# Performance work log

Measured on AMD Instinct MI355X. Metric: run time of the kernel, lower is better.

Reference implementation:

```python
import jax, jax.numpy as jnp
import numpy as np

B, T, C = 2, 1024, 1024
E, F, K = 8, 2048, 2


def setup_inputs() -> dict:
    key = jax.random.key(0)
    ks = jax.random.split(key, 5)
    s = 1.0 / np.sqrt(C)
    return {
        "x": jax.random.normal(ks[0], (B, T, C), jnp.float32),
        "Wr": jax.random.normal(ks[1], (E, C), jnp.float32) * s,   # router weight [E, d_model]
        "w1": jax.random.normal(ks[2], (E, C, F), jnp.float32) * s, # gate proj per expert
        "w3": jax.random.normal(ks[3], (E, C, F), jnp.float32) * s, # up proj per expert
        "w2": jax.random.normal(ks[4], (E, F, C), jnp.float32) * (1.0 / np.sqrt(F)),  # down proj
    }


def reference(x, Wr, w1, w3, w2):
    Bq, Tq, Cq = x.shape
    flat = x.reshape(-1, Cq)                          # [N, C]
    N = flat.shape[0]
    probs = jax.nn.softmax(flat @ Wr.T, axis=-1)      # [N, E]
    topw, topi = jax.lax.top_k(probs, K)              # [N, K]
    topw = topw / jnp.sum(topw, axis=-1, keepdims=True)
    # dense gate matrix: zero for unselected experts (same math as masked loop)
    gates = jnp.zeros((N, E), flat.dtype).at[jnp.arange(N)[:, None], topi].set(topw)
    # evaluate all experts, weight by gates (gate=0 kills unrouted experts)
    h1 = jnp.einsum('nd,edf->nef', flat, w1)          # [N, E, F]
    h3 = jnp.einsum('nd,edf->nef', flat, w3)
    h = jax.nn.silu(h1) * h3
    y = jnp.einsum('nef,efd->ned', h, w2)             # [N, E, C]
    out = jnp.einsum('ned,ne->nd', y, gates)          # [N, C]
    return out.reshape(Bq, Tq, Cq)
```

## Files before the change

### kernel.cpp

```cpp
#include <hip/hip_runtime.h>
#include <math.h>

typedef _Float16 f16;
typedef _Float16 f16x2 __attribute__((ext_vector_type(2)));
typedef _Float16 f16x4 __attribute__((ext_vector_type(4)));
typedef _Float16 f16x8 __attribute__((ext_vector_type(8)));
typedef __fp16 h16x2 __attribute__((ext_vector_type(2)));
typedef float f32x4 __attribute__((ext_vector_type(4)));
typedef float f32x16 __attribute__((ext_vector_type(16)));

#define N_TOK 2048
#define C_DIM 1024
#define E_NUM 8
#define F_DIM 2048
#define BM 256

#define WS_COUNTS    0
#define WS_OFFSETS   64
#define WS_CURSOR    192
#define WS_TOPI      256
#define WS_TOPW      (WS_TOPI + 16384)
#define WS_ROWS      (WS_TOPW + 16384)
#define WS_SLOT      (WS_ROWS + 16384)
#define WS_X16       (1ull << 20)
#define WS_H         (6ull << 20)
#define WS_Y0        (23ull << 20)
#define WS_Y1        (32ull << 20)

__device__ __forceinline__ f16x2 pkrtz(float a, float b) {
  union { h16x2 h; f16x2 f; } u;
  u.h = __builtin_amdgcn_cvt_pkrtz(a, b);
  return u.f;
}

__global__ void cvtx_kernel(const float* __restrict__ x, f16* __restrict__ x16) {
  int i = (blockIdx.x * 256 + threadIdx.x) * 8;
  f32x4 a = *(const f32x4*)(x + i);
  f32x4 b = *(const f32x4*)(x + i + 4);
  union { f16x8 v; f16x2 h[4]; } u;
  u.h[0] = pkrtz(a[0], a[1]);
  u.h[1] = pkrtz(a[2], a[3]);
  u.h[2] = pkrtz(b[0], b[1]);
  u.h[3] = pkrtz(b[2], b[3]);
  *(f16x8*)(x16 + i) = u.v;
}

__global__ void router_kernel(const float* __restrict__ x, const float* __restrict__ Wr,
                              int* counts, int* topi, float* topw) {
  int tok = blockIdx.x * 4 + (threadIdx.x >> 6);
  int lane = threadIdx.x & 63;
  const float* xr = x + (size_t)tok * C_DIM;
  float xv[16];
#pragma unroll
  for (int i = 0; i < 16; ++i) xv[i] = xr[i * 64 + lane];
  float logit[E_NUM];
#pragma unroll
  for (int e = 0; e < E_NUM; ++e) {
    const float* wr = Wr + (size_t)e * C_DIM;
    float acc = 0.f;
#pragma unroll
    for (int i = 0; i < 16; ++i) acc += xv[i] * wr[i * 64 + lane];
#pragma unroll
    for (int s = 1; s < 64; s <<= 1) acc += __shfl_xor(acc, s, 64);
    logit[e] = acc;
  }
  if (lane == 0) {
    float m = logit[0];
#pragma unroll
    for (int e = 1; e < E_NUM; ++e) m = fmaxf(m, logit[e]);
    float p[E_NUM];
#pragma unroll
    for (int e = 0; e < E_NUM; ++e) p[e] = expf(logit[e] - m);
    float p0 = -1.f, p1 = -1.f;
    int i0 = 0, i1 = 0;
#pragma unroll
    for (int e = 0; e < E_NUM; ++e) {
      float v = p[e];
      if (v > p0) { p1 = p0; i1 = i0; p0 = v; i0 = e; }
      else if (v > p1) { p1 = v; i1 = e; }
    }
    float inv = 1.f / (p0 + p1);
    topi[2 * tok] = i0; topi[2 * tok + 1] = i1;
    topw[2 * tok] = p0 * inv; topw[2 * tok + 1] = p1 * inv;
    atomicAdd(&counts[i0], 1);
    atomicAdd(&counts[i1], 1);
  }
}

__global__ void scan_kernel(const int* counts, int* offsets, int* cursor) {
  if (threadIdx.x == 0) {
    int o = 0;
    for (int e = 0; e < E_NUM; ++e) {
      offsets[e] = o; cursor[e] = o;
      o += counts[e];
    }
    offsets[E_NUM] = o;
  }
}

__global__ void scatter_kernel(const int* __restrict__ topi, int* cursor,
                               int* rows_perm, int* slot_of) {
  int n = blockIdx.x * blockDim.x + threadIdx.x;
  if (n >= N_TOK) return;
#pragma unroll
  for (int k = 0; k < 2; ++k) {
    int e = topi[2 * n + k];
    int pos = atomicAdd(&cursor[e], 1);
    rows_perm[pos] = n;
    slot_of[2 * n + k] = pos;
  }
}

#define BARRIER_PUB()                                          \
  asm volatile("s_waitcnt lgkmcnt(0)" ::: "memory");           \
  __builtin_amdgcn_s_barrier();                                \
  asm volatile("" ::: "memory");

#define UP_PACK_WRITE()                                                  \
  { union { f16x8 v; f16x2 h[4]; } u;                                    \
    u.h[0] = pkrtz(b1r[0], b1r[1]); u.h[1] = pkrtz(b1r[2], b1r[3]);      \
    u.h[2] = pkrtz(b1r[4], b1r[5]); u.h[3] = pkrtz(b1r[6], b1r[7]);      \
    *(f16x8*)&B1_lds[cur][bso] = u.v;                                    \
    u.h[0] = pkrtz(b3r[0], b3r[1]); u.h[1] = pkrtz(b3r[2], b3r[3]);      \
    u.h[2] = pkrtz(b3r[4], b3r[5]); u.h[3] = pkrtz(b3r[6], b3r[7]);      \
    *(f16x8*)&B3_lds[cur][bso] = u.v; }

#define UP_LOAD(ANXT, KN)                                                \
  { _Pragma("unroll") for (int j = 0; j < 8; ++j) {                      \
      b1r[j] = w1p[(size_t)(KN + j) * F_DIM];                            \
      b3r[j] = w3p[(size_t)(KN + j) * F_DIM]; }                          \
    _Pragma("unroll") for (int mi = 0; mi < 2; ++mi)                     \
      _Pragma("unroll") for (int kk = 0; kk < 2; ++kk)                   \
        ANXT[mi][kk] = *(const f16x8*)(aptr[mi] + (KN) + kk * 16 + fh * 8); }

#define UP_MFMA(ACUR)                                                    \
  { f16x8 bf[2][2];                                                      \
    _Pragma("unroll") for (int ni = 0; ni < 2; ++ni)                     \
      _Pragma("unroll") for (int kk = 0; kk < 2; ++kk) {                 \
        int col = wc + ni * 32 + ln31;                                   \
        int cell = (kk * 2 + fh) ^ ((col >> 1) & 3);                     \
        bf[ni][kk] = *(const f16x8*)&B1_lds[cur][col * 32 + cell * 8]; } \
    __builtin_amdgcn_s_setprio(1);                                       \
    _Pragma("unroll") for (int kk = 0; kk < 2; ++kk)                     \
      _Pragma("unroll") for (int mi = 0; mi < 2; ++mi)                   \
        _Pragma("unroll") for (int ni = 0; ni < 2; ++ni)                 \
          acc1[mi][ni] = __builtin_amdgcn_mfma_f32_32x32x16_f16(ACUR[mi][kk], bf[ni][kk], acc1[mi][ni], 0, 0, 0); \
    __builtin_amdgcn_s_setprio(0);                                       \
    _Pragma("unroll") for (int ni = 0; ni < 2; ++ni)                     \
      _Pragma("unroll") for (int kk = 0; kk < 2; ++kk) {                 \
        int col = wc + ni * 32 + ln31;                                   \
        int cell = (kk * 2 + fh) ^ ((col >> 1) & 3);                     \
        bf[ni][kk] = *(const f16x8*)&B3_lds[cur][col * 32 + cell * 8]; } \
    __builtin_amdgcn_s_setprio(1);                                       \
    _Pragma("unroll") for (int kk = 0; kk < 2; ++kk)                     \
      _Pragma("unroll") for (int mi = 0; mi < 2; ++mi)                   \
        _Pragma("unroll") for (int ni = 0; ni < 2; ++ni)                 \
          acc3[mi][ni] = __builtin_amdgcn_mfma_f32_32x32x16_f16(ACUR[mi][kk], bf[ni][kk], acc3[mi][ni], 0, 0, 0); \
    __builtin_amdgcn_s_setprio(0);                                       \
    cur ^= 1; }

#define UP_STEP(ACUR, ANXT, KN) \
  { UP_PACK_WRITE(); UP_LOAD(ANXT, KN); BARRIER_PUB(); UP_MFMA(ACUR); }

__launch_bounds__(512, 2)
__global__ void upproj_kernel(const f16* __restrict__ x16,
                              const float* __restrict__ w1,
                              const float* __restrict__ w3,
                              const int* __restrict__ counts,
                              const int* __restrict__ offsets,
                              const int* __restrict__ rows_perm,
                              f16* __restrict__ h_buf) {
  __shared__ __align__(16) f16 B1_lds[2][128 * 32];
  __shared__ __align__(16) f16 B3_lds[2][128 * 32];

  int bid = blockIdx.x;
  int e = bid & 7;
  int slot = bid >> 3;
  int fidx = slot & 15;
  int tile = slot >> 4;
  int cnt = counts[e];
  if (tile * BM >= cnt) return;
  int row0 = tile * BM;
  int off = offsets[e];
  int f0 = fidx * 128;
  int t = threadIdx.x, wid = t >> 6, lane = t & 63;
  int ln31 = lane & 31, fh = lane >> 5;
  int wr = (wid >> 1) * 64, wc = (wid & 1) * 64;

  const f16* aptr[2];
#pragma unroll
  for (int mi = 0; mi < 2; ++mi) {
    int lr = row0 + wr + mi * 32 + ln31;
    if (lr > cnt - 1) lr = cnt - 1;
    aptr[mi] = x16 + (size_t)rows_perm[off + lr] * C_DIM;
  }

  int bcol = t & 127, kg = t >> 7;
  int bso = bcol * 32 + ((kg ^ ((bcol >> 1) & 3)) * 8);
  const size_t eb = (size_t)e * C_DIM * F_DIM;
  const float* w1p = w1 + eb + (size_t)(kg * 8) * F_DIM + f0 + bcol;
  const float* w3p = w3 + eb + (size_t)(kg * 8) * F_DIM + f0 + bcol;

  f32x16 acc1[2][2] = {};
  f32x16 acc3[2][2] = {};
  float b1r[8], b3r[8];
  f16x8 aX[2][2], aY[2][2];
  int cur = 0;

  UP_LOAD(aX, 0);
  for (int tp = 0; tp < 15; ++tp) {
    UP_STEP(aX, aY, (2 * tp + 1) * 32);
    UP_STEP(aY, aX, (2 * tp + 2) * 32);
  }
  UP_STEP(aX, aY, 31 * 32);
  { UP_PACK_WRITE(); BARRIER_PUB(); UP_MFMA(aY); }

#pragma unroll
  for (int mi = 0; mi < 2; ++mi)
#pragma unroll
    for (int ni = 0; ni < 2; ++ni)
#pragma unroll
      for (int i = 0; i < 16; ++i) {
        int rr = (i & 3) + 8 * (i >> 2) + 4 * fh;
        int lr = row0 + wr + mi * 32 + rr;
        if (lr < cnt) {
          float v1 = acc1[mi][ni][i], v3 = acc3[mi][ni][i];
          float hval = v1 / (1.f + expf(-v1)) * v3;
          h_buf[(size_t)(off + lr) * F_DIM + f0 + wc + ni * 32 + ln31] = (f16)hval;
        }
      }
}

#define DN_PACK_WRITE()                                                  \
  { union { f16x8 v; f16x2 h[4]; } u;                                    \
    u.h[0] = pkrtz(br[0], br[1]); u.h[1] = pkrtz(br[2], br[3]);          \
    u.h[2] = pkrtz(br[4], br[5]); u.h[3] = pkrtz(br[6], br[7]);          \
    *(f16x8*)&B_lds[cur][bso] = u.v; }

#define DN_LOAD(ANXT, KN)                                                \
  { _Pragma("unroll") for (int j = 0; j < 8; ++j)                        \
      br[j] = w2p[(size_t)(KN + j) * C_DIM];                             \
    _Pragma("unroll") for (int mi = 0; mi < 2; ++mi)                     \
      _Pragma("unroll") for (int kk = 0; kk < 2; ++kk)                   \
        ANXT[mi][kk] = *(const f16x8*)(aptr[mi] + (KN) + kk * 16 + fh * 8); }

#define DN_MFMA(ACUR)                                                    \
  { f16x8 bf[2][2];                                                      \
    _Pragma("unroll") for (int ni = 0; ni < 2; ++ni)                     \
      _Pragma("unroll") for (int kk = 0; kk < 2; ++kk) {                 \
        int col = wc + ni * 32 + ln31;                                   \
        int cell = (kk * 2 + fh) ^ ((col >> 1) & 3);                     \
        bf[ni][kk] = *(const f16x8*)&B_lds[cur][col * 32 + cell * 8]; }  \
    __builtin_amdgcn_s_setprio(1);                                       \
    _Pragma("unroll") for (int kk = 0; kk < 2; ++kk)                     \
      _Pragma("unroll") for (int mi = 0; mi < 2; ++mi)                   \
        _Pragma("unroll") for (int ni = 0; ni < 2; ++ni)                 \
          acc[mi][ni] = __builtin_amdgcn_mfma_f32_32x32x16_f16(ACUR[mi][kk], bf[ni][kk], acc[mi][ni], 0, 0, 0); \
    __builtin_amdgcn_s_setprio(0);                                       \
    cur ^= 1; }

#define DN_STEP(ACUR, ANXT, KN) \
  { DN_PACK_WRITE(); DN_LOAD(ANXT, KN); BARRIER_PUB(); DN_MFMA(ACUR); }

__launch_bounds__(512, 2)
__global__ void downproj_kernel(const f16* __restrict__ h_buf,
                                const float* __restrict__ w2,
                                const int* __restrict__ counts,
                                const int* __restrict__ offsets,
                                f16* __restrict__ y0,
                                f16* __restrict__ y1) {
  __shared__ __align__(16) f16 B_lds[2][128 * 32];

  int bid = blockIdx.x;
  int e = bid & 7;
  int slot = bid >> 3;
  int cidx = slot & 7;
  int kh = (slot >> 3) & 1;
  int tile = slot >> 4;
  int cnt = counts[e];
  if (tile * BM >= cnt) return;
  f16* yb = kh ? y1 : y0;
  int row0 = tile * BM;
  int off = offsets[e];
  int c0 = cidx * 128;
  int t = threadIdx.x, wid = t >> 6, lane = t & 63;
  int ln31 = lane & 31, fh = lane >> 5;
  int wr = (wid >> 1) * 64, wc = (wid & 1) * 64;

  const f16* aptr[2];
#pragma unroll
  for (int mi = 0; mi < 2; ++mi) {
    int lr = row0 + wr + mi * 32 + ln31;
    if (lr > cnt - 1) lr = cnt - 1;
    aptr[mi] = h_buf + (size_t)(off + lr) * F_DIM + kh * 1024;
  }

  int bcol = t & 127, kg = t >> 7;
  int bso = bcol * 32 + ((kg ^ ((bcol >> 1) & 3)) * 8);
  const float* w2p = w2 + (size_t)e * F_DIM * C_DIM
                     + (size_t)(kh * 1024 + kg * 8) * C_DIM + c0 + bcol;

  f32x16 acc[2][2] = {};
  float br[8];
  f16x8 aX[2][2], aY[2][2];
  int cur = 0;

  DN_LOAD(aX, 0);
  for (int tp = 0; tp < 15; ++tp) {
    DN_STEP(aX, aY, (2 * tp + 1) * 32);
    DN_STEP(aY, aX, (2 * tp + 2) * 32);
  }
  DN_STEP(aX, aY, 31 * 32);
  { DN_PACK_WRITE(); BARRIER_PUB(); DN_MFMA(aY); }

#pragma unroll
  for (int mi = 0; mi < 2; ++mi)
#pragma unroll
    for (int ni = 0; ni < 2; ++ni)
#pragma unroll
      for (int i = 0; i < 16; ++i) {
        int rr = (i & 3) + 8 * (i >> 2) + 4 * fh;
        int lr = row0 + wr + mi * 32 + rr;
        if (lr < cnt)
          yb[(size_t)(off + lr) * C_DIM + c0 + wc + ni * 32 + ln31] = (f16)acc[mi][ni][i];
      }
}

__global__ void combine_kernel(const f16* __restrict__ y0, const f16* __restrict__ y1,
                               const int* __restrict__ slot_of,
                               const float* __restrict__ topw,
                               float* __restrict__ out) {
  int n = blockIdx.x;
  int s0 = slot_of[2 * n], s1 = slot_of[2 * n + 1];
  float g0 = topw[2 * n], g1 = topw[2 * n + 1];
  int c = threadIdx.x * 4;
  f16x4 a0 = *(const f16x4*)(y0 + (size_t)s0 * C_DIM + c);
  f16x4 a1 = *(const f16x4*)(y1 + (size_t)s0 * C_DIM + c);
  f16x4 b0 = *(const f16x4*)(y0 + (size_t)s1 * C_DIM + c);
  f16x4 b1 = *(const f16x4*)(y1 + (size_t)s1 * C_DIM + c);
  f32x4 o;
#pragma unroll
  for (int i = 0; i < 4; ++i)
    o[i] = g0 * ((float)a0[i] + (float)a1[i]) + g1 * ((float)b0[i] + (float)b1[i]);
  *(f32x4*)(out + (size_t)n * C_DIM + c) = o;
}

extern "C" void kernel_launch(void* const* d_in, const int* in_sizes, int n_in,
                              void* d_out, int out_size, void* d_ws, size_t ws_size,
                              hipStream_t stream) {
  const float* x  = (const float*)d_in[0];
  const float* Wr = (const float*)d_in[1];
  const float* w1 = (const float*)d_in[2];
  const float* w3 = (const float*)d_in[3];
  const float* w2 = (const float*)d_in[4];
  float* out = (float*)d_out;
  char* ws = (char*)d_ws;

  int* counts    = (int*)(ws + WS_COUNTS);
  int* offsets   = (int*)(ws + WS_OFFSETS);
  int* cursor    = (int*)(ws + WS_CURSOR);
  int* topi      = (int*)(ws + WS_TOPI);
  float* topw    = (float*)(ws + WS_TOPW);
  int* rows_perm = (int*)(ws + WS_ROWS);
  int* slot_of   = (int*)(ws + WS_SLOT);
  f16* x16       = (f16*)(ws + WS_X16);
  f16* h_buf     = (f16*)(ws + WS_H);
  f16* y0        = (f16*)(ws + WS_Y0);
  f16* y1        = (f16*)(ws + WS_Y1);

  (void)hipMemsetAsync(ws, 0, 256, stream);
  cvtx_kernel<<<N_TOK * C_DIM / 8 / 256, 256, 0, stream>>>(x, x16);
  router_kernel<<<N_TOK / 4, 256, 0, stream>>>(x, Wr, counts, topi, topw);
  scan_kernel<<<1, 64, 0, stream>>>(counts, offsets, cursor);
  scatter_kernel<<<N_TOK / 256, 256, 0, stream>>>(topi, cursor, rows_perm, slot_of);
  upproj_kernel<<<E_NUM * 128, 512, 0, stream>>>(
      x16, w1, w3, counts, offsets, rows_perm, h_buf);
  downproj_kernel<<<E_NUM * 128, 512, 0, stream>>>(
      h_buf, w2, counts, offsets, y0, y1);
  combine_kernel<<<N_TOK, 256, 0, stream>>>(y0, y1, slot_of, topw, out);
}
```

Before: 234.7 us.

## Stage A tiles via global_load_lds triple buffering with smaller 128x64 tiles

The up and down projection GEMMs now load activation tiles straight into LDS with global_load_lds into a triple-buffered, swizzled layout. Weight loads are issued two steps ahead, and the code waits on vmcnt counts instead of holding A fragments in registers. Tiles shrink from 256x128 with 512 threads to 128x64 with 256 threads, and the grid grows fourfold to raise occupancy and cut padding waste for small expert counts. The trade-off is that the fp32 weights are re-read from global memory by more blocks, and the explicit vmcnt counts must match the exact number of issued loads.

```diff
diff --git a/kernel.cpp b/kernel.cpp
--- a/kernel.cpp
+++ b/kernel.cpp
@@ -13,7 +13,7 @@
 #define C_DIM 1024
 #define E_NUM 8
 #define F_DIM 2048
-#define BM 256
+#define BM 128
 
 #define WS_COUNTS    0
 #define WS_OFFSETS   64
@@ -27,6 +27,11 @@
 #define WS_Y0        (23ull << 20)
 #define WS_Y1        (32ull << 20)
 
+__device__ __forceinline__ void glds16(const void* g, void* l) {
+  __builtin_amdgcn_global_load_lds((const __attribute__((address_space(1))) void*)g,
+                                   (__attribute__((address_space(3))) void*)l, 16, 0, 0);
+}
+
 __device__ __forceinline__ f16x2 pkrtz(float a, float b) {
   union { h16x2 h; f16x2 f; } u;
   u.h = __builtin_amdgcn_cvt_pkrtz(a, b);
@@ -111,58 +116,51 @@
   }
 }
 
-#define BARRIER_PUB()                                          \
-  asm volatile("s_waitcnt lgkmcnt(0)" ::: "memory");           \
-  __builtin_amdgcn_s_barrier();                                \
-  asm volatile("" ::: "memory");
-
-#define UP_PACK_WRITE()                                                  \
-  { union { f16x8 v; f16x2 h[4]; } u;                                    \
-    u.h[0] = pkrtz(b1r[0], b1r[1]); u.h[1] = pkrtz(b1r[2], b1r[3]);      \
-    u.h[2] = pkrtz(b1r[4], b1r[5]); u.h[3] = pkrtz(b1r[6], b1r[7]);      \
-    *(f16x8*)&B1_lds[cur][bso] = u.v;                                    \
-    u.h[0] = pkrtz(b3r[0], b3r[1]); u.h[1] = pkrtz(b3r[2], b3r[3]);      \
-    u.h[2] = pkrtz(b3r[4], b3r[5]); u.h[3] = pkrtz(b3r[6], b3r[7]);      \
-    *(f16x8*)&B3_lds[cur][bso] = u.v; }
-
-#define UP_LOAD(ANXT, KN)                                                \
-  { _Pragma("unroll") for (int j = 0; j < 8; ++j) {                      \
-      b1r[j] = w1p[(size_t)(KN + j) * F_DIM];                            \
-      b3r[j] = w3p[(size_t)(KN + j) * F_DIM]; }                          \
-    _Pragma("unroll") for (int mi = 0; mi < 2; ++mi)                     \
-      _Pragma("unroll") for (int kk = 0; kk < 2; ++kk)                   \
-        ANXT[mi][kk] = *(const f16x8*)(aptr[mi] + (KN) + kk * 16 + fh * 8); }
-
-#define UP_MFMA(ACUR)                                                    \
-  { f16x8 bf[2][2];                                                      \
-    _Pragma("unroll") for (int ni = 0; ni < 2; ++ni)                     \
-      _Pragma("unroll") for (int kk = 0; kk < 2; ++kk) {                 \
-        int col = wc + ni * 32 + ln31;                                   \
-        int cell = (kk * 2 + fh) ^ ((col >> 1) & 3);                     \
-        bf[ni][kk] = *(const f16x8*)&B1_lds[cur][col * 32 + cell * 8]; } \
-    __builtin_amdgcn_s_setprio(1);                                       \
-    _Pragma("unroll") for (int kk = 0; kk < 2; ++kk)                     \
-      _Pragma("unroll") for (int mi = 0; mi < 2; ++mi)                   \
-        _Pragma("unroll") for (int ni = 0; ni < 2; ++ni)                 \
-          acc1[mi][ni] = __builtin_amdgcn_mfma_f32_32x32x16_f16(ACUR[mi][kk], bf[ni][kk], acc1[mi][ni], 0, 0, 0); \
-    __builtin_amdgcn_s_setprio(0);                                       \
-    _Pragma("unroll") for (int ni = 0; ni < 2; ++ni)                     \
-      _Pragma("unroll") for (int kk = 0; kk < 2; ++kk) {                 \
-        int col = wc + ni * 32 + ln31;                                   \
-        int cell = (kk * 2 + fh) ^ ((col >> 1) & 3);                     \
-        bf[ni][kk] = *(const f16x8*)&B3_lds[cur][col * 32 + cell * 8]; } \
-    __builtin_amdgcn_s_setprio(1);                                       \
-    _Pragma("unroll") for (int kk = 0; kk < 2; ++kk)                     \
-      _Pragma("unroll") for (int mi = 0; mi < 2; ++mi)                   \
-        _Pragma("unroll") for (int ni = 0; ni < 2; ++ni)                 \
-          acc3[mi][ni] = __builtin_amdgcn_mfma_f32_32x32x16_f16(ACUR[mi][kk], bf[ni][kk], acc3[mi][ni], 0, 0, 0); \
-    __builtin_amdgcn_s_setprio(0);                                       \
-    cur ^= 1; }
-
-#define UP_STEP(ACUR, ANXT, KN) \
-  { UP_PACK_WRITE(); UP_LOAD(ANXT, KN); BARRIER_PUB(); UP_MFMA(ACUR); }
-
-__launch_bounds__(512, 2)
+#define ROT3(P0, P1, P2) { f16* _t = P0; P0 = P1; P1 = P2; P2 = _t; }
+
+#define UP_ISSUE(B1R, B3R, KN)                                     \
+  { _Pragma("unroll") for (int j = 0; j < 8; ++j) {                \
+      B1R[j] = w1p[(size_t)((KN) + j) * F_DIM];                    \
+      B3R[j] = w3p[(size_t)((KN) + j) * F_DIM]; }                  \
+    glds16(asrc[0] + (KN), a_f + (wid * 64) * 8);                  \
+    glds16(asrc[1] + (KN), a_f + (256 + wid * 64) * 8); }
+
+#define UP_STEP(B1R, B3R, BUF, T, ISSUE, VM)                                   \
+  { asm volatile("s_waitcnt vmcnt(" #VM ")" ::: "memory");                     \
+    { union { f16x8 v; f16x2 h[4]; } u;                                        \
+      u.h[0] = pkrtz(B1R[0], B1R[1]); u.h[1] = pkrtz(B1R[2], B1R[3]);          \
+      u.h[2] = pkrtz(B1R[4], B1R[5]); u.h[3] = pkrtz(B1R[6], B1R[7]);          \
+      *(f16x8*)(B1_lds[BUF] + t * 8) = u.v;                                    \
+      u.h[0] = pkrtz(B3R[0], B3R[1]); u.h[1] = pkrtz(B3R[2], B3R[3]);          \
+      u.h[2] = pkrtz(B3R[4], B3R[5]); u.h[3] = pkrtz(B3R[6], B3R[7]);          \
+      *(f16x8*)(B3_lds[BUF] + t * 8) = u.v; }                                  \
+    asm volatile("s_waitcnt lgkmcnt(0)" ::: "memory");                         \
+    __builtin_amdgcn_s_barrier();                                              \
+    asm volatile("" ::: "memory");                                             \
+    if (ISSUE) { UP_ISSUE(B1R, B3R, ((T) + 2) * 32); }                         \
+    { f16x8 af[2][2], bf[2];                                                   \
+      _Pragma("unroll") for (int mi = 0; mi < 2; ++mi)                         \
+        _Pragma("unroll") for (int kk = 0; kk < 2; ++kk) {                     \
+          int row = wr + mi * 32 + ln31;                                       \
+          int cell = (kk * 2 + fh) ^ ((row >> 1) & 3);                         \
+          af[mi][kk] = *(const f16x8*)&a_c[row * 32 + cell * 8]; }             \
+      _Pragma("unroll") for (int kk = 0; kk < 2; ++kk)                         \
+        bf[kk] = *(const f16x8*)(B1_lds[BUF] + ((kk * 2 + fh) * 64 + wc + ln31) * 8); \
+      __builtin_amdgcn_s_setprio(1);                                           \
+      _Pragma("unroll") for (int kk = 0; kk < 2; ++kk)                         \
+        _Pragma("unroll") for (int mi = 0; mi < 2; ++mi)                       \
+          acc1[mi] = __builtin_amdgcn_mfma_f32_32x32x16_f16(af[mi][kk], bf[kk], acc1[mi], 0, 0, 0); \
+      __builtin_amdgcn_s_setprio(0);                                           \
+      _Pragma("unroll") for (int kk = 0; kk < 2; ++kk)                         \
+        bf[kk] = *(const f16x8*)(B3_lds[BUF] + ((kk * 2 + fh) * 64 + wc + ln31) * 8); \
+      __builtin_amdgcn_s_setprio(1);                                           \
+      _Pragma("unroll") for (int kk = 0; kk < 2; ++kk)                         \
+        _Pragma("unroll") for (int mi = 0; mi < 2; ++mi)                       \
+          acc3[mi] = __builtin_amdgcn_mfma_f32_32x32x16_f16(af[mi][kk], bf[kk], acc3[mi], 0, 0, 0); \
+      __builtin_amdgcn_s_setprio(0); }                                         \
+    ROT3(a_c, a_n, a_f); }
+
+__launch_bounds__(256, 3)
 __global__ void upproj_kernel(const f16* __restrict__ x16,
                               const float* __restrict__ w1,
                               const float* __restrict__ w3,
@@ -170,160 +168,158 @@
                               const int* __restrict__ offsets,
                               const int* __restrict__ rows_perm,
                               f16* __restrict__ h_buf) {
-  __shared__ __align__(16) f16 B1_lds[2][128 * 32];
-  __shared__ __align__(16) f16 B3_lds[2][128 * 32];
+  __shared__ __align__(16) f16 A_lds[3][BM * 32];
+  __shared__ __align__(16) f16 B1_lds[2][4 * 64 * 8];
+  __shared__ __align__(16) f16 B3_lds[2][4 * 64 * 8];
 
   int bid = blockIdx.x;
   int e = bid & 7;
   int slot = bid >> 3;
-  int fidx = slot & 15;
-  int tile = slot >> 4;
+  int fidx = slot & 31;
+  int tile = slot >> 5;
   int cnt = counts[e];
   if (tile * BM >= cnt) return;
   int row0 = tile * BM;
   int off = offsets[e];
-  int f0 = fidx * 128;
+  int f0 = fidx * 64;
   int t = threadIdx.x, wid = t >> 6, lane = t & 63;
   int ln31 = lane & 31, fh = lane >> 5;
-  int wr = (wid >> 1) * 64, wc = (wid & 1) * 64;
-
-  const f16* aptr[2];
-#pragma unroll
-  for (int mi = 0; mi < 2; ++mi) {
-    int lr = row0 + wr + mi * 32 + ln31;
-    if (lr > cnt - 1) lr = cnt - 1;
-    aptr[mi] = x16 + (size_t)rows_perm[off + lr] * C_DIM;
-  }
-
-  int bcol = t & 127, kg = t >> 7;
-  int bso = bcol * 32 + ((kg ^ ((bcol >> 1) & 3)) * 8);
+  int wr = (wid >> 1) * 64, wc = (wid & 1) * 32;
+
+  const f16* asrc[2];
+#pragma unroll
+  for (int p = 0; p < 2; ++p) {
+    int c = p * 256 + t;
+    int row = c >> 2, cc = c & 3;
+    int lr = row0 + row; if (lr > cnt - 1) lr = cnt - 1;
+    asrc[p] = x16 + (size_t)rows_perm[off + lr] * C_DIM + 8 * (cc ^ ((row >> 1) & 3));
+  }
+
   const size_t eb = (size_t)e * C_DIM * F_DIM;
-  const float* w1p = w1 + eb + (size_t)(kg * 8) * F_DIM + f0 + bcol;
-  const float* w3p = w3 + eb + (size_t)(kg * 8) * F_DIM + f0 + bcol;
-
-  f32x16 acc1[2][2] = {};
-  f32x16 acc3[2][2] = {};
-  float b1r[8], b3r[8];
-  f16x8 aX[2][2], aY[2][2];
-  int cur = 0;
-
-  UP_LOAD(aX, 0);
+  const float* w1p = w1 + eb + (size_t)((t >> 6) * 8) * F_DIM + f0 + (t & 63);
+  const float* w3p = w3 + eb + (size_t)((t >> 6) * 8) * F_DIM + f0 + (t & 63);
+
+  f32x16 acc1[2] = {};
+  f32x16 acc3[2] = {};
+  float b1X[8], b3X[8], b1Y[8], b3Y[8];
+
+  f16 *a_c = &A_lds[0][0], *a_n = &A_lds[1][0], *a_f = &A_lds[2][0];
+
+  { f16* sv = a_f; a_f = a_c; UP_ISSUE(b1X, b3X, 0); a_f = a_n; UP_ISSUE(b1Y, b3Y, 32); a_f = sv; }
+
   for (int tp = 0; tp < 15; ++tp) {
-    UP_STEP(aX, aY, (2 * tp + 1) * 32);
-    UP_STEP(aY, aX, (2 * tp + 2) * 32);
-  }
-  UP_STEP(aX, aY, 31 * 32);
-  { UP_PACK_WRITE(); BARRIER_PUB(); UP_MFMA(aY); }
+    UP_STEP(b1X, b3X, 0, 2 * tp, 1, 18);
+    UP_STEP(b1Y, b3Y, 1, 2 * tp + 1, 1, 18);
+  }
+  UP_STEP(b1X, b3X, 0, 30, 0, 18);
+  UP_STEP(b1Y, b3Y, 1, 31, 0, 0);
 
 #pragma unroll
   for (int mi = 0; mi < 2; ++mi)
 #pragma unroll
-    for (int ni = 0; ni < 2; ++ni)
-#pragma unroll
-      for (int i = 0; i < 16; ++i) {
-        int rr = (i & 3) + 8 * (i >> 2) + 4 * fh;
-        int lr = row0 + wr + mi * 32 + rr;
-        if (lr < cnt) {
-          float v1 = acc1[mi][ni][i], v3 = acc3[mi][ni][i];
-          float hval = v1 / (1.f + expf(-v1)) * v3;
-          h_buf[(size_t)(off + lr) * F_DIM + f0 + wc + ni * 32 + ln31] = (f16)hval;
-        }
+    for (int i = 0; i < 16; ++i) {
+      int rr = (i & 3) + 8 * (i >> 2) + 4 * fh;
+      int lr = row0 + wr + mi * 32 + rr;
+      if (lr < cnt) {
+        float v1 = acc1[mi][i], v3 = acc3[mi][i];
+        float hval = v1 / (1.f + expf(-v1)) * v3;
+        h_buf[(size_t)(off + lr) * F_DIM + f0 + wc + ln31] = (f16)hval;
       }
-}
-
-#define DN_PACK_WRITE()                                                  \
-  { union { f16x8 v; f16x2 h[4]; } u;                                    \
-    u.h[0] = pkrtz(br[0], br[1]); u.h[1] = pkrtz(br[2], br[3]);          \
-    u.h[2] = pkrtz(br[4], br[5]); u.h[3] = pkrtz(br[6], br[7]);          \
-    *(f16x8*)&B_lds[cur][bso] = u.v; }
-
-#define DN_LOAD(ANXT, KN)                                                \
-  { _Pragma("unroll") for (int j = 0; j < 8; ++j)                        \
-      br[j] = w2p[(size_t)(KN + j) * C_DIM];                             \
-    _Pragma("unroll") for (int mi = 0; mi < 2; ++mi)                     \
-      _Pragma("unroll") for (int kk = 0; kk < 2; ++kk)                   \
-        ANXT[mi][kk] = *(const f16x8*)(aptr[mi] + (KN) + kk * 16 + fh * 8); }
-
-#define DN_MFMA(ACUR)                                                    \
-  { f16x8 bf[2][2];                                                      \
-    _Pragma("unroll") for (int ni = 0; ni < 2; ++ni)                     \
-      _Pragma("unroll") for (int kk = 0; kk < 2; ++kk) {                 \
-        int col = wc + ni * 32 + ln31;                                   \
-        int cell = (kk * 2 + fh) ^ ((col >> 1) & 3);                     \
-        bf[ni][kk] = *(const f16x8*)&B_lds[cur][col * 32 + cell * 8]; }  \
-    __builtin_amdgcn_s_setprio(1);                                       \
-    _Pragma("unroll") for (int kk = 0; kk < 2; ++kk)                     \
-      _Pragma("unroll") for (int mi = 0; mi < 2; ++mi)                   \
-        _Pragma("unroll") for (int ni = 0; ni < 2; ++ni)                 \
-          acc[mi][ni] = __builtin_amdgcn_mfma_f32_32x32x16_f16(ACUR[mi][kk], bf[ni][kk], acc[mi][ni], 0, 0, 0); \
-    __builtin_amdgcn_s_setprio(0);                                       \
-    cur ^= 1; }
-
-#define DN_STEP(ACUR, ANXT, KN) \
-  { DN_PACK_WRITE(); DN_LOAD(ANXT, KN); BARRIER_PUB(); DN_MFMA(ACUR); }
-
-__launch_bounds__(512, 2)
+    }
+}
+
+#define DN_ISSUE(BR, KN)                                           \
+  { _Pragma("unroll") for (int j = 0; j < 8; ++j)                  \
+      BR[j] = w2p[(size_t)((KN) + j) * C_DIM];                     \
+    glds16(asrc[0] + (KN), a_f + (wid * 64) * 8);                  \
+    glds16(asrc[1] + (KN), a_f + (256 + wid * 64) * 8); }
+
+#define DN_STEP(BR, BUF, T, ISSUE, VM)                                         \
+  { asm volatile("s_waitcnt vmcnt(" #VM ")" ::: "memory");                     \
+    { union { f16x8 v; f16x2 h[4]; } u;                                        \
+      u.h[0] = pkrtz(BR[0], BR[1]); u.h[1] = pkrtz(BR[2], BR[3]);              \
+      u.h[2] = pkrtz(BR[4], BR[5]); u.h[3] = pkrtz(BR[6], BR[7]);              \
+      *(f16x8*)(B_lds[BUF] + t * 8) = u.v; }                                   \
+    asm volatile("s_waitcnt lgkmcnt(0)" ::: "memory");                         \
+    __builtin_amdgcn_s_barrier();                                              \
+    asm volatile("" ::: "memory");                                             \
+    if (ISSUE) { DN_ISSUE(BR, ((T) + 2) * 32); }                               \
+    { f16x8 af[2][2], bf[2];                                                   \
+      _Pragma("unroll") for (int mi = 0; mi < 2; ++mi)                         \
+        _Pragma("unroll") for (int kk = 0; kk < 2; ++kk) {                     \
+          int row = wr + mi * 32 + ln31;                                       \
+          int cell = (kk * 2 + fh) ^ ((row >> 1) & 3);                         \
+          af[mi][kk] = *(const f16x8*)&a_c[row * 32 + cell * 8]; }             \
+      _Pragma("unroll") for (int kk = 0; kk < 2; ++kk)                         \
+        bf[kk] = *(const f16x8*)(B_lds[BUF] + ((kk * 2 + fh) * 64 + wc + ln31) * 8); \
+      __builtin_amdgcn_s_setprio(1);                                           \
+      _Pragma("unroll") for (int kk = 0; kk < 2; ++kk)                         \
+        _Pragma("unroll") for (int mi = 0; mi < 2; ++mi)                       \
+          acc[mi] = __builtin_amdgcn_mfma_f32_32x32x16_f16(af[mi][kk], bf[kk], acc[mi], 0, 0, 0); \
+      __builtin_amdgcn_s_setprio(0); }                                         \
+    ROT3(a_c, a_n, a_f); }
+
+__launch_bounds__(256, 3)
 __global__ void downproj_kernel(const f16* __restrict__ h_buf,
                                 const float* __restrict__ w2,
                                 const int* __restrict__ counts,
                                 const int* __restrict__ offsets,
                                 f16* __restrict__ y0,
                                 f16* __restrict__ y1) {
-  __shared__ __align__(16) f16 B_lds[2][128 * 32];
+  __shared__ __align__(16) f16 A_lds[3][BM * 32];
+  __shared__ __align__(16) f16 B_lds[2][4 * 64 * 8];
 
   int bid = blockIdx.x;
   int e = bid & 7;
   int slot = bid >> 3;
-  int cidx = slot & 7;
-  int kh = (slot >> 3) & 1;
-  int tile = slot >> 4;
+  int cidx = slot & 15;
+  int kh = (slot >> 4) & 1;
+  int tile = slot >> 5;
   int cnt = counts[e];
   if (tile * BM >= cnt) return;
   f16* yb = kh ? y1 : y0;
   int row0 = tile * BM;
   int off = offsets[e];
-  int c0 = cidx * 128;
+  int c0 = cidx * 64;
   int t = threadIdx.x, wid = t >> 6, lane = t & 63;
   int ln31 = lane & 31, fh = lane >> 5;
-  int wr = (wid >> 1) * 64, wc = (wid & 1) * 64;
-
-  const f16* aptr[2];
-#pragma unroll
-  for (int mi = 0; mi < 2; ++mi) {
-    int lr = row0 + wr + mi * 32 + ln31;
-    if (lr > cnt - 1) lr = cnt - 1;
-    aptr[mi] = h_buf + (size_t)(off + lr) * F_DIM + kh * 1024;
-  }
-
-  int bcol = t & 127, kg = t >> 7;
-  int bso = bcol * 32 + ((kg ^ ((bcol >> 1) & 3)) * 8);
+  int wr = (wid >> 1) * 64, wc = (wid & 1) * 32;
+
+  const f16* asrc[2];
+#pragma unroll
+  for (int p = 0; p < 2; ++p) {
+    int c = p * 256 + t;
+    int row = c >> 2, cc = c & 3;
+    int lr = row0 + row; if (lr > cnt - 1) lr = cnt - 1;
+    asrc[p] = h_buf + (size_t)(off + lr) * F_DIM + kh * 1024 + 8 * (cc ^ ((row >> 1) & 3));
+  }
+
   const float* w2p = w2 + (size_t)e * F_DIM * C_DIM
-                     + (size_t)(kh * 1024 + kg * 8) * C_DIM + c0 + bcol;
-
-  f32x16 acc[2][2] = {};
-  float br[8];
-  f16x8 aX[2][2], aY[2][2];
-  int cur = 0;
-
-  DN_LOAD(aX, 0);
+                     + (size_t)(kh * 1024 + (t >> 6) * 8) * C_DIM + c0 + (t & 63);
+
+  f32x16 acc[2] = {};
+  float bX[8], bY[8];
+
+  f16 *a_c = &A_lds[0][0], *a_n = &A_lds[1][0], *a_f = &A_lds[2][0];
+
+  { f16* sv = a_f; a_f = a_c; DN_ISSUE(bX, 0); a_f = a_n; DN_ISSUE(bY, 32); a_f = sv; }
+
   for (int tp = 0; tp < 15; ++tp) {
-    DN_STEP(aX, aY, (2 * tp + 1) * 32);
-    DN_STEP(aY, aX, (2 * tp + 2) * 32);
-  }
-  DN_STEP(aX, aY, 31 * 32);
-  { DN_PACK_WRITE(); BARRIER_PUB(); DN_MFMA(aY); }
+    DN_STEP(bX, 0, 2 * tp, 1, 10);
+    DN_STEP(bY, 1, 2 * tp + 1, 1, 10);
+  }
+  DN_STEP(bX, 0, 30, 0, 10);
+  DN_STEP(bY, 1, 31, 0, 0);
 
 #pragma unroll
   for (int mi = 0; mi < 2; ++mi)
 #pragma unroll
-    for (int ni = 0; ni < 2; ++ni)
-#pragma unroll
-      for (int i = 0; i < 16; ++i) {
-        int rr = (i & 3) + 8 * (i >> 2) + 4 * fh;
-        int lr = row0 + wr + mi * 32 + rr;
-        if (lr < cnt)
-          yb[(size_t)(off + lr) * C_DIM + c0 + wc + ni * 32 + ln31] = (f16)acc[mi][ni][i];
-      }
+    for (int i = 0; i < 16; ++i) {
+      int rr = (i & 3) + 8 * (i >> 2) + 4 * fh;
+      int lr = row0 + wr + mi * 32 + rr;
+      if (lr < cnt)
+        yb[(size_t)(off + lr) * C_DIM + c0 + wc + ln31] = (f16)acc[mi][i];
+    }
 }
 
 __global__ void combine_kernel(const f16* __restrict__ y0, const f16* __restrict__ y1,
@@ -373,9 +369,9 @@
   router_kernel<<<N_TOK / 4, 256, 0, stream>>>(x, Wr, counts, topi, topw);
   scan_kernel<<<1, 64, 0, stream>>>(counts, offsets, cursor);
   scatter_kernel<<<N_TOK / 256, 256, 0, stream>>>(topi, cursor, rows_perm, slot_of);
-  upproj_kernel<<<E_NUM * 128, 512, 0, stream>>>(
+  upproj_kernel<<<E_NUM * 512, 256, 0, stream>>>(
       x16, w1, w3, counts, offsets, rows_perm, h_buf);
-  downproj_kernel<<<E_NUM * 128, 512, 0, stream>>>(
+  downproj_kernel<<<E_NUM * 512, 256, 0, stream>>>(
       h_buf, w2, counts, offsets, y0, y1);
   combine_kernel<<<N_TOK, 256, 0, stream>>>(y0, y1, slot_of, topw, out);
 }
```

Result: faster. 220.6 us (-6.0%).
